# Kernel tuning notes

Measured on AMD Instinct MI355X. Metric: run time of the kernel, lower is better.

## Reference

```python
import jax, jax.numpy as jnp
import numpy as np

N_NODES = 100000
N_EDGES = 1600000
IN_FEATS = 128
HIDDEN = 128
OUT_DIM = 128


def setup_inputs() -> dict:
    key = jax.random.key(0)
    ks = jax.random.split(key, 8)
    x = jax.random.normal(ks[0], (N_NODES, IN_FEATS), dtype=jnp.float32)
    W1 = jax.random.normal(ks[1], (IN_FEATS, HIDDEN), dtype=jnp.float32) * (1.0 / np.sqrt(IN_FEATS))
    b1 = jnp.zeros((HIDDEN,), dtype=jnp.float32)
    W2 = jax.random.normal(ks[2], (HIDDEN, HIDDEN), dtype=jnp.float32) * (1.0 / np.sqrt(HIDDEN))
    b2 = jnp.zeros((HIDDEN,), dtype=jnp.float32)
    W3 = jax.random.normal(ks[3], (HIDDEN, OUT_DIM), dtype=jnp.float32) * (1.0 / np.sqrt(HIDDEN))
    b3 = jnp.zeros((OUT_DIM,), dtype=jnp.float32)
    edge_src = jax.random.randint(ks[4], (N_EDGES,), 0, N_NODES, dtype=jnp.int32)
    edge_dst = jax.random.randint(ks[5], (N_EDGES,), 0, N_NODES, dtype=jnp.int32)
    return {"x": x, "W1": W1, "b1": b1, "W2": W2, "b2": b2, "W3": W3, "b3": b3,
            "edge_src": edge_src, "edge_dst": edge_dst}


def _mean_agg(h, edge_src, edge_dst, inv_deg):
    # gather src features, scatter-sum to dst, divide by in-degree (mean)
    summed = jax.ops.segment_sum(h[edge_src], edge_dst, num_segments=N_NODES)
    return summed * inv_deg[:, None]


def reference(x, W1, b1, W2, b2, W3, b3, edge_src, edge_dst):
    # in-degree (clamped to 1 to avoid div-by-zero, matching mean over empty = 0)
    deg = jax.ops.segment_sum(jnp.ones((N_EDGES,), dtype=jnp.float32), edge_dst,
                              num_segments=N_NODES)
    inv_deg = 1.0 / jnp.maximum(deg, 1.0)

    # DGL GINConv (eps=0, mean): h = Linear(h + mean_neighbors(h))
    h = x
    h = (h + _mean_agg(h, edge_src, edge_dst, inv_deg)) @ W1 + b1
    h = jax.nn.relu(h)  # dropout inactive in eval mode
    h = (h + _mean_agg(h, edge_src, edge_dst, inv_deg)) @ W2 + b2
    h = jax.nn.relu(h)
    h = (h + _mean_agg(h, edge_src, edge_dst, inv_deg)) @ W3 + b3
    return h
```

## Files before the change

### kernel.cpp

```cpp
#include <hip/hip_runtime.h>
#include <hip/hip_bf16.h>
#include <stdint.h>

#if __has_builtin(__builtin_amdgcn_cvt_pk_f32_fp8) && __has_builtin(__builtin_amdgcn_cvt_pk_fp8_f32)
#define FP8_HW 1
#else
#define FP8_HW 0
#include <hip/hip_fp8.h>
#endif

#define N_NODES 100000
#define N_EDGES 1600000
#define FEAT 128

#define BKT_SHIFT 8
#define BKT_SIZE  256
#define NB_BKT    391
#define BKT_CAP   5664
#define NB_SC     800
#define EPB_SC    2000

typedef uint16_t u16;
typedef uint32_t u32;
typedef __attribute__((ext_vector_type(8))) short bf16x8;
typedef __attribute__((ext_vector_type(4))) float f32x4;
typedef __attribute__((ext_vector_type(2))) float f32x2;

__device__ __forceinline__ u16 bf16_rn(float f){
  u32 u = __float_as_uint(f);
  u += 0x7FFFu + ((u >> 16) & 1u);
  return (u16)(u >> 16);
}
__device__ __forceinline__ float bf16_lo(u32 p){ return __uint_as_float(p << 16); }
__device__ __forceinline__ float bf16_hi(u32 p){ return __uint_as_float(p & 0xFFFF0000u); }

__device__ __forceinline__ void fp8x4_to_f32(u32 w, float* o){
#if FP8_HW
  f32x2 a = __builtin_amdgcn_cvt_pk_f32_fp8(w, false);
  f32x2 b = __builtin_amdgcn_cvt_pk_f32_fp8(w, true);
  o[0] = a.x; o[1] = a.y; o[2] = b.x; o[3] = b.y;
#else
  #pragma unroll
  for (int i = 0; i < 4; ++i){
    __hip_fp8_e4m3 t; t.__x = (uint8_t)((w >> (8 * i)) & 0xFF);
    o[i] = (float)t;
  }
#endif
}
__device__ __forceinline__ u32 f32x4_to_fp8(float a, float b, float c, float d){
#if FP8_HW
  u32 r = __builtin_amdgcn_cvt_pk_fp8_f32(a, b, 0, false);
  r = __builtin_amdgcn_cvt_pk_fp8_f32(c, d, r, true);
  return r;
#else
  __hip_fp8_e4m3 qa(a), qb(b), qc(c), qd(d);
  return (u32)qa.__x | ((u32)qb.__x << 8) | ((u32)qc.__x << 16) | ((u32)qd.__x << 24);
#endif
}


__global__ __launch_bounds__(512) void hist_kernel(const int* __restrict__ dst,
                                                   int* __restrict__ hcnt){
  __shared__ int h[NB_BKT];
  for (int i = threadIdx.x; i < NB_BKT; i += 512) h[i] = 0;
  __syncthreads();
  int base = blockIdx.x * EPB_SC;
  for (int e = base + threadIdx.x; e < base + EPB_SC; e += 512)
    atomicAdd(&h[dst[e] >> BKT_SHIFT], 1);
  __syncthreads();
  for (int i = threadIdx.x; i < NB_BKT; i += 512)
    hcnt[blockIdx.x * NB_BKT + i] = h[i];
}

__global__ void hscan_kernel(int* __restrict__ hcnt, int* __restrict__ cursor){
  __shared__ int s[256];
  int b = blockIdx.x, t = threadIdx.x;
  int v[4]; int sum = 0;
  #pragma unroll
  for (int j = 0; j < 4; ++j){
    int blk = 4 * t + j;
    v[j] = (blk < NB_SC) ? hcnt[blk * NB_BKT + b] : 0;
    sum += v[j];
  }
  s[t] = sum;
  __syncthreads();
  for (int d = 1; d < 256; d <<= 1){
    int add = (t >= d) ? s[t - d] : 0;
    __syncthreads();
    s[t] += add;
    __syncthreads();
  }
  int excl = s[t] - sum;
  #pragma unroll
  for (int j = 0; j < 4; ++j){
    int blk = 4 * t + j;
    if (blk < NB_SC){ hcnt[blk * NB_BKT + b] = excl; excl += v[j]; }
  }
  if (t == 255) cursor[b] = s[255];
}

__global__ __launch_bounds__(512) void scatter_kernel(const int* __restrict__ src,
                                                      const int* __restrict__ dst,
                                                      const int* __restrict__ hcnt,
                                                      uint2* __restrict__ bbuf){
  __shared__ int cur[NB_BKT];
  for (int i = threadIdx.x; i < NB_BKT; i += 512)
    cur[i] = hcnt[blockIdx.x * NB_BKT + i];
  __syncthreads();
  int base = blockIdx.x * EPB_SC;
  for (int e = base + threadIdx.x; e < base + EPB_SC; e += 512){
    int d = dst[e];
    int b = d >> BKT_SHIFT;
    int p = atomicAdd(&cur[b], 1);
    bbuf[(size_t)b * BKT_CAP + p] = make_uint2((u32)src[e], (u32)(d & (BKT_SIZE - 1)));
  }
}

__global__ __launch_bounds__(1024) void csr_build_kernel(const uint2* __restrict__ bbuf,
                                 const int* __restrict__ cursor,
                                 int* __restrict__ offs, int* __restrict__ deg,
                                 float* __restrict__ inv_deg, int* __restrict__ eidx){
  __shared__ int hist[BKT_SIZE];
  __shared__ int s[BKT_SIZE];
  __shared__ int cu[BKT_SIZE];
  int b = blockIdx.x;
  int t = threadIdx.x;
  int lo = b * BKT_CAP;
  int hi = lo + cursor[b];
  if (t < BKT_SIZE) hist[t] = 0;
  __syncthreads();
  for (int e = lo + t; e < hi; e += 1024)
    atomicAdd(&hist[bbuf[e].y], 1);
  __syncthreads();
  int v = 0, pv = 0;
  if (t < BKT_SIZE){
    v  = hist[t];
    pv = (v + 7) & ~7;
    s[t] = pv;
  }
  __syncthreads();
  for (int d = 1; d < BKT_SIZE; d <<= 1){
    int add = (t < BKT_SIZE && t >= d) ? s[t - d] : 0;
    __syncthreads();
    if (t < BKT_SIZE && t >= d) s[t] += add;
    __syncthreads();
  }
  if (t < BKT_SIZE){
    int excl = s[t] - pv;
    int node = b * BKT_SIZE + t;
    if (node < N_NODES){
      offs[node]    = lo + excl;
      deg[node]     = v;
      inv_deg[node] = 1.0f / fmaxf((float)v, 1.0f);
      for (int p = v; p < pv; ++p) eidx[lo + excl + p] = 0;
    }
    s[t]  = excl;
    cu[t] = 0;
  }
  __syncthreads();
  for (int e = lo + t; e < hi; e += 1024){
    uint2 q = bbuf[e];
    int p = atomicAdd(&cu[q.y], 1);
    eidx[lo + s[q.y] + p] = (int)q.x;
  }
}


__global__ void cvt_x8_kernel(const float* __restrict__ x, uint2* __restrict__ X8){
  int i = blockIdx.x * 256 + threadIdx.x;
  const float4* p = (const float4*)x + (size_t)i * 2;
  float4 a = p[0], b = p[1];
  uint2 o;
  o.x = f32x4_to_fp8(a.x, a.y, a.z, a.w);
  o.y = f32x4_to_fp8(b.x, b.y, b.z, b.w);
  X8[i] = o;
}

__global__ void wprep3_kernel(const float* __restrict__ W1, const float* __restrict__ W2,
                              const float* __restrict__ W3, u16* __restrict__ Wp1,
                              u16* __restrict__ Wp2, u16* __restrict__ Wp3){
  int which = blockIdx.x >> 6;
  int b     = blockIdx.x & 63;
  const float* W = (which == 0) ? W1 : (which == 1) ? W2 : W3;
  u16*        Wp = (which == 0) ? Wp1 : (which == 1) ? Wp2 : Wp3;
  int idx = b * 256 + threadIdx.x;
  int j    = idx & 7;
  int lane = (idx >> 3) & 63;
  int t    = idx >> 9;
  int k0 = t & 3, n0 = t >> 2;
  int k = k0 * 32 + (lane >> 4) * 8 + j;
  int n = n0 * 16 + (lane & 15);
  Wp[idx] = bf16_rn(W[k * FEAT + n]);
}


template<int SM, int OUT>
__global__ __launch_bounds__(64, 8) void layer_kernel(
    const u32* __restrict__ n8,
    const u16* __restrict__ hb,
    const float* __restrict__ xf,
    const int* __restrict__ offs,
    const int* __restrict__ deg,
    const float* __restrict__ inv_deg,
    const int* __restrict__ eidx,
    const u16* __restrict__ Wp,
    const float* __restrict__ bias,
    u16* __restrict__ Hout,
    u32* __restrict__ H8out,
    float* __restrict__ Fout){
  __shared__ u16 Tt[16 * FEAT];
  const int tid   = threadIdx.x;
  const int nsub  = tid >> 4;
  const int slice = tid & 15;
  const int base  = blockIdx.x * 16;

  for (int g = 0; g < 4; ++g){
    const int rrow = (g << 2) + nsub;
    const int node = base + rrow;
    const int start = offs[node];
    const int cnt   = deg[node];
    const int* ep = eidx + start;
    const int pcnt = (cnt + 7) & ~7;

    float acc[8];
    #pragma unroll
    for (int j = 0; j < 8; ++j) acc[j] = 0.f;

    uint4 qa = make_uint4(0,0,0,0), qb = qa;
    if (pcnt > 0){ qa = *(const uint4*)ep; qb = *(const uint4*)(ep + 4); }

    for (int e = 0; e < pcnt; e += 8){
      uint4 qa2 = *(const uint4*)(ep + e + 8);
      uint4 qb2 = *(const uint4*)(ep + e + 12);
      uint2 r0 = *(const uint2*)(n8 + (size_t)qa.x * 32 + slice * 2);
      uint2 r1 = *(const uint2*)(n8 + (size_t)qa.y * 32 + slice * 2);
      uint2 r2 = *(const uint2*)(n8 + (size_t)qa.z * 32 + slice * 2);
      uint2 r3 = *(const uint2*)(n8 + (size_t)qa.w * 32 + slice * 2);
      uint2 r4 = *(const uint2*)(n8 + (size_t)qb.x * 32 + slice * 2);
      uint2 r5 = *(const uint2*)(n8 + (size_t)qb.y * 32 + slice * 2);
      uint2 r6 = *(const uint2*)(n8 + (size_t)qb.z * 32 + slice * 2);
      uint2 r7 = *(const uint2*)(n8 + (size_t)qb.w * 32 + slice * 2);
      float t0[4], t1[4];
      #define ACC8(rr) \
        fp8x4_to_f32(rr.x, t0); fp8x4_to_f32(rr.y, t1); \
        acc[0]+=t0[0]; acc[1]+=t0[1]; acc[2]+=t0[2]; acc[3]+=t0[3]; \
        acc[4]+=t1[0]; acc[5]+=t1[1]; acc[6]+=t1[2]; acc[7]+=t1[3];
      ACC8(r0) ACC8(r1) ACC8(r2) ACC8(r3) ACC8(r4) ACC8(r5) ACC8(r6) ACC8(r7)
      #undef ACC8
      qa = qa2; qb = qb2;
    }

    if (pcnt > cnt){
      float f = (float)(pcnt - cnt);
      uint2 rz = *(const uint2*)(n8 + slice * 2);
      float t0[4], t1[4];
      fp8x4_to_f32(rz.x, t0); fp8x4_to_f32(rz.y, t1);
      acc[0]-=f*t0[0]; acc[1]-=f*t0[1]; acc[2]-=f*t0[2]; acc[3]-=f*t0[3];
      acc[4]-=f*t1[0]; acc[5]-=f*t1[1]; acc[6]-=f*t1[2]; acc[7]-=f*t1[3];
    }

    const float w = inv_deg[node];
    float self[8];
    if (SM == 1){
      const float* sp = xf + (size_t)node * FEAT + slice * 8;
      float4 a = *(const float4*)sp;
      float4 b = *(const float4*)(sp + 4);
      self[0]=a.x; self[1]=a.y; self[2]=a.z; self[3]=a.w;
      self[4]=b.x; self[5]=b.y; self[6]=b.z; self[7]=b.w;
    } else {
      const u16* sp = hb + (size_t)node * FEAT + slice * 8;
      uint4 s0 = *(const uint4*)sp;
      self[0]=bf16_lo(s0.x); self[1]=bf16_hi(s0.x); self[2]=bf16_lo(s0.y); self[3]=bf16_hi(s0.y);
      self[4]=bf16_lo(s0.z); self[5]=bf16_hi(s0.z); self[6]=bf16_lo(s0.w); self[7]=bf16_hi(s0.w);
    }
    uint4 o;
    o.x = (u32)bf16_rn(self[0] + w*acc[0]) | ((u32)bf16_rn(self[1] + w*acc[1]) << 16);
    o.y = (u32)bf16_rn(self[2] + w*acc[2]) | ((u32)bf16_rn(self[3] + w*acc[3]) << 16);
    o.z = (u32)bf16_rn(self[4] + w*acc[4]) | ((u32)bf16_rn(self[5] + w*acc[5]) << 16);
    o.w = (u32)bf16_rn(self[6] + w*acc[6]) | ((u32)bf16_rn(self[7] + w*acc[7]) << 16);
    ((uint4*)Tt)[rrow * 16 + (slice ^ (rrow & 7))] = o;
  }
  __syncthreads();

  const int quad = tid >> 4;
  const int c    = tid & 15;

  bf16x8 A[4];
  #pragma unroll
  for (int k0 = 0; k0 < 4; ++k0){
    uint4 t = ((const uint4*)Tt)[c * 16 + ((quad + k0 * 4) ^ (c & 7))];
    A[k0] = *(const bf16x8*)&t;
  }
  if (OUT == 0) __syncthreads();

  #pragma unroll
  for (int h = 0; h < 2; ++h){
    f32x4 acc2[4];
    #pragma unroll
    for (int i = 0; i < 4; ++i) acc2[i] = (f32x4){0.f, 0.f, 0.f, 0.f};
    #pragma unroll
    for (int i = 0; i < 4; ++i){
      int n0 = h * 4 + i;
      #pragma unroll
      for (int k0 = 0; k0 < 4; ++k0){
        bf16x8 b = *(const bf16x8*)(Wp + (size_t)(((n0 << 2) | k0) * 64 + tid) * 8);
        acc2[i] = __builtin_amdgcn_mfma_f32_16x16x32_bf16(A[k0], b, acc2[i], 0, 0, 0);
      }
    }
    #pragma unroll
    for (int i = 0; i < 4; ++i){
      int n0 = h * 4 + i;
      float bv = bias[n0 * 16 + c];
      #pragma unroll
      for (int r = 0; r < 4; ++r){
        int rr  = quad * 4 + r;
        int col = n0 * 16 + c;
        if (OUT == 1){
          Fout[(size_t)(base + rr) * FEAT + col] = acc2[i][r] + bv;
        } else {
          float v = fmaxf(acc2[i][r] + bv, 0.f);
          Tt[rr * FEAT + (col ^ ((rr & 7) << 3))] = bf16_rn(v);
        }
      }
    }
  }

  if (OUT == 0){
    __syncthreads();
    #pragma unroll
    for (int it = 0; it < 4; ++it){
      int p  = it * 64 + tid;
      int rr = p >> 4, qq = p & 15;
      int node = base + rr;
      uint4 d = ((const uint4*)Tt)[rr * 16 + (qq ^ (rr & 7))];
      *(uint4*)(Hout + (size_t)node * FEAT + qq * 8) = d;
      uint2 o8;
      o8.x = f32x4_to_fp8(bf16_lo(d.x), bf16_hi(d.x), bf16_lo(d.y), bf16_hi(d.y));
      o8.y = f32x4_to_fp8(bf16_lo(d.z), bf16_hi(d.z), bf16_lo(d.w), bf16_hi(d.w));
      *(uint2*)(H8out + (size_t)node * 32 + qq * 2) = o8;
    }
  }
}


static inline size_t align_up(size_t x){ return (x + 255) & ~(size_t)255; }

extern "C" void kernel_launch(void* const* d_in, const int* in_sizes, int n_in,
                              void* d_out, int out_size, void* d_ws, size_t ws_size,
                              hipStream_t stream){
  const float* x  = (const float*)d_in[0];
  const float* W1 = (const float*)d_in[1];
  const float* b1 = (const float*)d_in[2];
  const float* W2 = (const float*)d_in[3];
  const float* b2 = (const float*)d_in[4];
  const float* W3 = (const float*)d_in[5];
  const float* b3 = (const float*)d_in[6];
  const int* esrc = (const int*)d_in[7];
  const int* edst = (const int*)d_in[8];

  char* w = (char*)d_ws;
  int*   deg     = (int*)w;    w += align_up((size_t)N_NODES * 4);
  int*   offs    = (int*)w;    w += align_up((size_t)N_NODES * 4);
  float* inv_deg = (float*)w;  w += align_up((size_t)N_NODES * 4);
  int*   eidx    = (int*)w;    w += align_up((size_t)NB_BKT * BKT_CAP * 4);
  u16*   Wp1     = (u16*)w;    w += align_up((size_t)16384 * 2);
  u16*   Wp2     = (u16*)w;    w += align_up((size_t)16384 * 2);
  u16*   Wp3     = (u16*)w;    w += align_up((size_t)16384 * 2);
  u16*   Hb      = (u16*)w;    w += align_up((size_t)N_NODES * FEAT * 2);
  u32*   H8b     = (u32*)w;    w += align_up((size_t)N_NODES * 32 * 4);

  uint2* bbuf   = (uint2*)Hb;
  int*   cursor = (int*)H8b;
  int*   hcnt   = (int*)((char*)H8b + align_up((size_t)NB_BKT * 4));

  u16* Ha  = (u16*)d_out;
  u32* H8a = (u32*)((char*)d_out + (size_t)N_NODES * FEAT * 2);
  u32* X8  = (u32*)((char*)d_out + (size_t)N_NODES * FEAT * 3);

  hist_kernel<<<NB_SC, 512, 0, stream>>>(edst, hcnt);
  hscan_kernel<<<NB_BKT, 256, 0, stream>>>(hcnt, cursor);
  scatter_kernel<<<NB_SC, 512, 0, stream>>>(esrc, edst, hcnt, bbuf);
  csr_build_kernel<<<NB_BKT, 1024, 0, stream>>>(bbuf, cursor, offs, deg, inv_deg, eidx);

  wprep3_kernel<<<192, 256, 0, stream>>>(W1, W2, W3, Wp1, Wp2, Wp3);
  cvt_x8_kernel<<<N_EDGES / 256, 256, 0, stream>>>(x, (uint2*)X8);

  const int LAYER_BLOCKS = N_NODES / 16;

  layer_kernel<1, 0><<<LAYER_BLOCKS, 64, 0, stream>>>(
      X8, (const u16*)nullptr, x, offs, deg, inv_deg, eidx, Wp1, b1,
      Ha, H8a, (float*)nullptr);

  layer_kernel<0, 0><<<LAYER_BLOCKS, 64, 0, stream>>>(
      H8a, Ha, (const float*)nullptr, offs, deg, inv_deg, eidx, Wp2, b2,
      Hb, H8b, (float*)nullptr);

  layer_kernel<0, 1><<<LAYER_BLOCKS, 64, 0, stream>>>(
      H8b, Hb, (const float*)nullptr, offs, deg, inv_deg, eidx, Wp3, b3,
      (u16*)nullptr, (u32*)nullptr, (float*)d_out);

  (void)in_sizes; (void)n_in; (void)out_size; (void)ws_size; (void)w;
}
```

Baseline: 302.7 us.

## Use two waves per layer block and software-pipeline neighbor row gathers

Each layer block now runs 128 threads as two wavefronts. Each wave aggregates 8 of the 16 nodes and computes half of the output columns in the MFMA stage, instead of one wave doing all of it. The gather loop is double-buffered: the fp8 rows for the next 8 edges are loaded before the current 8 are accumulated, so memory latency can overlap with the conversion work. Accumulation uses packed f32x2 fp8 conversion adds. The cost is more registers per thread for the in-flight rows and an extra speculative index load past each node's edge list.

```diff
diff --git a/kernel.cpp b/kernel.cpp
--- a/kernel.cpp
+++ b/kernel.cpp
@@ -55,6 +55,20 @@
 #else
   __hip_fp8_e4m3 qa(a), qb(b), qc(c), qd(d);
   return (u32)qa.__x | ((u32)qb.__x << 8) | ((u32)qc.__x << 16) | ((u32)qd.__x << 24);
+#endif
+}
+
+__device__ __forceinline__ void acc_row(uint2 r, f32x2* acc){
+#if FP8_HW
+  acc[0] += __builtin_amdgcn_cvt_pk_f32_fp8(r.x, false);
+  acc[1] += __builtin_amdgcn_cvt_pk_f32_fp8(r.x, true);
+  acc[2] += __builtin_amdgcn_cvt_pk_f32_fp8(r.y, false);
+  acc[3] += __builtin_amdgcn_cvt_pk_f32_fp8(r.y, true);
+#else
+  float t0[4], t1[4];
+  fp8x4_to_f32(r.x, t0); fp8x4_to_f32(r.y, t1);
+  acc[0].x += t0[0]; acc[0].y += t0[1]; acc[1].x += t0[2]; acc[1].y += t0[3];
+  acc[2].x += t1[0]; acc[2].y += t1[1]; acc[3].x += t1[2]; acc[3].y += t1[3];
 #endif
 }
 
@@ -195,7 +209,7 @@
 
 
 template<int SM, int OUT>
-__global__ __launch_bounds__(64, 8) void layer_kernel(
+__global__ __launch_bounds__(128, 8) void layer_kernel(
     const u32* __restrict__ n8,
     const u16* __restrict__ hb,
     const float* __restrict__ xf,
@@ -210,53 +224,70 @@
     float* __restrict__ Fout){
   __shared__ u16 Tt[16 * FEAT];
   const int tid   = threadIdx.x;
-  const int nsub  = tid >> 4;
-  const int slice = tid & 15;
+  const int wid   = tid >> 6;
+  const int lane  = tid & 63;
+  const int nsub  = lane >> 4;
+  const int slice = lane & 15;
   const int base  = blockIdx.x * 16;
-
-  for (int g = 0; g < 4; ++g){
-    const int rrow = (g << 2) + nsub;
+  const u32* gbase = n8 + slice * 2;
+
+  for (int g = 0; g < 2; ++g){
+    const int rrow = wid * 8 + (g << 2) + nsub;
     const int node = base + rrow;
     const int start = offs[node];
     const int cnt   = deg[node];
+    const int pcnt  = (cnt + 7) & ~7;
     const int* ep = eidx + start;
-    const int pcnt = (cnt + 7) & ~7;
-
-    float acc[8];
+
+    f32x2 acc[4];
     #pragma unroll
-    for (int j = 0; j < 8; ++j) acc[j] = 0.f;
-
-    uint4 qa = make_uint4(0,0,0,0), qb = qa;
-    if (pcnt > 0){ qa = *(const uint4*)ep; qb = *(const uint4*)(ep + 4); }
+    for (int j = 0; j < 4; ++j) acc[j] = (f32x2){0.f, 0.f};
+
+    uint2 rc[8];
+    #pragma unroll
+    for (int j = 0; j < 8; ++j) rc[j] = make_uint2(0u, 0u);
+    if (pcnt > 0){
+      uint4 q0 = *(const uint4*)ep;
+      uint4 q1 = *(const uint4*)(ep + 4);
+      rc[0] = *(const uint2*)(gbase + (size_t)q0.x * 32);
+      rc[1] = *(const uint2*)(gbase + (size_t)q0.y * 32);
+      rc[2] = *(const uint2*)(gbase + (size_t)q0.z * 32);
+      rc[3] = *(const uint2*)(gbase + (size_t)q0.w * 32);
+      rc[4] = *(const uint2*)(gbase + (size_t)q1.x * 32);
+      rc[5] = *(const uint2*)(gbase + (size_t)q1.y * 32);
+      rc[6] = *(const uint2*)(gbase + (size_t)q1.z * 32);
+      rc[7] = *(const uint2*)(gbase + (size_t)q1.w * 32);
+    }
+    uint4 qn1 = *(const uint4*)(ep + 8);
+    uint4 qn2 = *(const uint4*)(ep + 12);
 
     for (int e = 0; e < pcnt; e += 8){
-      uint4 qa2 = *(const uint4*)(ep + e + 8);
-      uint4 qb2 = *(const uint4*)(ep + e + 12);
-      uint2 r0 = *(const uint2*)(n8 + (size_t)qa.x * 32 + slice * 2);
-      uint2 r1 = *(const uint2*)(n8 + (size_t)qa.y * 32 + slice * 2);
-      uint2 r2 = *(const uint2*)(n8 + (size_t)qa.z * 32 + slice * 2);
-      uint2 r3 = *(const uint2*)(n8 + (size_t)qa.w * 32 + slice * 2);
-      uint2 r4 = *(const uint2*)(n8 + (size_t)qb.x * 32 + slice * 2);
-      uint2 r5 = *(const uint2*)(n8 + (size_t)qb.y * 32 + slice * 2);
-      uint2 r6 = *(const uint2*)(n8 + (size_t)qb.z * 32 + slice * 2);
-      uint2 r7 = *(const uint2*)(n8 + (size_t)qb.w * 32 + slice * 2);
-      float t0[4], t1[4];
-      #define ACC8(rr) \
-        fp8x4_to_f32(rr.x, t0); fp8x4_to_f32(rr.y, t1); \
-        acc[0]+=t0[0]; acc[1]+=t0[1]; acc[2]+=t0[2]; acc[3]+=t0[3]; \
-        acc[4]+=t1[0]; acc[5]+=t1[1]; acc[6]+=t1[2]; acc[7]+=t1[3];
-      ACC8(r0) ACC8(r1) ACC8(r2) ACC8(r3) ACC8(r4) ACC8(r5) ACC8(r6) ACC8(r7)
-      #undef ACC8
-      qa = qa2; qb = qb2;
+      uint2 rn[8];
+      rn[0] = *(const uint2*)(gbase + (size_t)qn1.x * 32);
+      rn[1] = *(const uint2*)(gbase + (size_t)qn1.y * 32);
+      rn[2] = *(const uint2*)(gbase + (size_t)qn1.z * 32);
+      rn[3] = *(const uint2*)(gbase + (size_t)qn1.w * 32);
+      rn[4] = *(const uint2*)(gbase + (size_t)qn2.x * 32);
+      rn[5] = *(const uint2*)(gbase + (size_t)qn2.y * 32);
+      rn[6] = *(const uint2*)(gbase + (size_t)qn2.z * 32);
+      rn[7] = *(const uint2*)(gbase + (size_t)qn2.w * 32);
+      qn1 = *(const uint4*)(ep + e + 16);
+      qn2 = *(const uint4*)(ep + e + 20);
+      #pragma unroll
+      for (int j = 0; j < 8; ++j) acc_row(rc[j], acc);
+      #pragma unroll
+      for (int j = 0; j < 8; ++j) rc[j] = rn[j];
     }
 
     if (pcnt > cnt){
       float f = (float)(pcnt - cnt);
-      uint2 rz = *(const uint2*)(n8 + slice * 2);
-      float t0[4], t1[4];
-      fp8x4_to_f32(rz.x, t0); fp8x4_to_f32(rz.y, t1);
-      acc[0]-=f*t0[0]; acc[1]-=f*t0[1]; acc[2]-=f*t0[2]; acc[3]-=f*t0[3];
-      acc[4]-=f*t1[0]; acc[5]-=f*t1[1]; acc[6]-=f*t1[2]; acc[7]-=f*t1[3];
+      uint2 rz = *(const uint2*)gbase;
+      f32x2 z[4];
+      #pragma unroll
+      for (int j = 0; j < 4; ++j) z[j] = (f32x2){0.f, 0.f};
+      acc_row(rz, z);
+      #pragma unroll
+      for (int j = 0; j < 4; ++j) acc[j] -= f * z[j];
     }
 
     const float w = inv_deg[node];
@@ -274,16 +305,16 @@
       self[4]=bf16_lo(s0.z); self[5]=bf16_hi(s0.z); self[6]=bf16_lo(s0.w); self[7]=bf16_hi(s0.w);
     }
     uint4 o;
-    o.x = (u32)bf16_rn(self[0] + w*acc[0]) | ((u32)bf16_rn(self[1] + w*acc[1]) << 16);
-    o.y = (u32)bf16_rn(self[2] + w*acc[2]) | ((u32)bf16_rn(self[3] + w*acc[3]) << 16);
-    o.z = (u32)bf16_rn(self[4] + w*acc[4]) | ((u32)bf16_rn(self[5] + w*acc[5]) << 16);
-    o.w = (u32)bf16_rn(self[6] + w*acc[6]) | ((u32)bf16_rn(self[7] + w*acc[7]) << 16);
+    o.x = (u32)bf16_rn(self[0] + w*acc[0].x) | ((u32)bf16_rn(self[1] + w*acc[0].y) << 16);
+    o.y = (u32)bf16_rn(self[2] + w*acc[1].x) | ((u32)bf16_rn(self[3] + w*acc[1].y) << 16);
+    o.z = (u32)bf16_rn(self[4] + w*acc[2].x) | ((u32)bf16_rn(self[5] + w*acc[2].y) << 16);
+    o.w = (u32)bf16_rn(self[6] + w*acc[3].x) | ((u32)bf16_rn(self[7] + w*acc[3].y) << 16);
     ((uint4*)Tt)[rrow * 16 + (slice ^ (rrow & 7))] = o;
   }
   __syncthreads();
 
-  const int quad = tid >> 4;
-  const int c    = tid & 15;
+  const int quad = lane >> 4;
+  const int c    = lane & 15;
 
   bf16x8 A[4];
   #pragma unroll
@@ -293,34 +324,31 @@
   }
   if (OUT == 0) __syncthreads();
 
-  #pragma unroll
-  for (int h = 0; h < 2; ++h){
-    f32x4 acc2[4];
+  f32x4 acc2[4];
+  #pragma unroll
+  for (int i = 0; i < 4; ++i) acc2[i] = (f32x4){0.f, 0.f, 0.f, 0.f};
+  #pragma unroll
+  for (int i = 0; i < 4; ++i){
+    int n0 = wid * 4 + i;
     #pragma unroll
-    for (int i = 0; i < 4; ++i) acc2[i] = (f32x4){0.f, 0.f, 0.f, 0.f};
+    for (int k0 = 0; k0 < 4; ++k0){
+      bf16x8 b = *(const bf16x8*)(Wp + (size_t)(((n0 << 2) | k0) * 64 + lane) * 8);
+      acc2[i] = __builtin_amdgcn_mfma_f32_16x16x32_bf16(A[k0], b, acc2[i], 0, 0, 0);
+    }
+  }
+  #pragma unroll
+  for (int i = 0; i < 4; ++i){
+    int n0 = wid * 4 + i;
+    float bv = bias[n0 * 16 + c];
     #pragma unroll
-    for (int i = 0; i < 4; ++i){
-      int n0 = h * 4 + i;
-      #pragma unroll
-      for (int k0 = 0; k0 < 4; ++k0){
-        bf16x8 b = *(const bf16x8*)(Wp + (size_t)(((n0 << 2) | k0) * 64 + tid) * 8);
-        acc2[i] = __builtin_amdgcn_mfma_f32_16x16x32_bf16(A[k0], b, acc2[i], 0, 0, 0);
-      }
-    }
-    #pragma unroll
-    for (int i = 0; i < 4; ++i){
-      int n0 = h * 4 + i;
-      float bv = bias[n0 * 16 + c];
-      #pragma unroll
-      for (int r = 0; r < 4; ++r){
-        int rr  = quad * 4 + r;
-        int col = n0 * 16 + c;
-        if (OUT == 1){
-          Fout[(size_t)(base + rr) * FEAT + col] = acc2[i][r] + bv;
-        } else {
-          float v = fmaxf(acc2[i][r] + bv, 0.f);
-          Tt[rr * FEAT + (col ^ ((rr & 7) << 3))] = bf16_rn(v);
-        }
+    for (int r = 0; r < 4; ++r){
+      int rr  = quad * 4 + r;
+      int col = n0 * 16 + c;
+      if (OUT == 1){
+        Fout[(size_t)(base + rr) * FEAT + col] = acc2[i][r] + bv;
+      } else {
+        float v = fmaxf(acc2[i][r] + bv, 0.f);
+        Tt[rr * FEAT + (col ^ ((rr & 7) << 3))] = bf16_rn(v);
       }
     }
   }
@@ -328,8 +356,8 @@
   if (OUT == 0){
     __syncthreads();
     #pragma unroll
-    for (int it = 0; it < 4; ++it){
-      int p  = it * 64 + tid;
+    for (int it = 0; it < 2; ++it){
+      int p  = it * 128 + tid;
       int rr = p >> 4, qq = p & 15;
       int node = base + rr;
       uint4 d = ((const uint4*)Tt)[rr * 16 + (qq ^ (rr & 7))];
@@ -387,15 +415,15 @@
 
   const int LAYER_BLOCKS = N_NODES / 16;
 
-  layer_kernel<1, 0><<<LAYER_BLOCKS, 64, 0, stream>>>(
+  layer_kernel<1, 0><<<LAYER_BLOCKS, 128, 0, stream>>>(
       X8, (const u16*)nullptr, x, offs, deg, inv_deg, eidx, Wp1, b1,
       Ha, H8a, (float*)nullptr);
 
-  layer_kernel<0, 0><<<LAYER_BLOCKS, 64, 0, stream>>>(
+  layer_kernel<0, 0><<<LAYER_BLOCKS, 128, 0, stream>>>(
       H8a, Ha, (const float*)nullptr, offs, deg, inv_deg, eidx, Wp2, b2,
       Hb, H8b, (float*)nullptr);
 
-  layer_kernel<0, 1><<<LAYER_BLOCKS, 64, 0, stream>>>(
+  layer_kernel<0, 1><<<LAYER_BLOCKS, 128, 0, stream>>>(
       H8b, Hb, (const float*)nullptr, offs, deg, inv_deg, eidx, Wp3, b3,
       (u16*)nullptr, (u32*)nullptr, (float*)d_out);
 
```

New measurement: 302.4 us. Within noise of the previous version (-0.1%).
